# Optimization experiments

Hardware: AMD Instinct MI355X
Metric: run time of the kernel (lower is better)

## Reference

```python
import jax, jax.numpy as jnp
import numpy as np

D_IN = 2048
D_SAE = 32768
K = 64


def setup_inputs() -> dict:
    key = jax.random.key(0)
    k1, k2, k3 = jax.random.split(key, 3)
    x = jax.random.normal(k1, (4096, D_IN), dtype=jnp.float32)
    # kaiming-uniform-style init
    bound_enc = float(np.sqrt(6.0 / D_IN))
    W_enc = jax.random.uniform(k2, (D_SAE, D_IN), jnp.float32, -bound_enc, bound_enc)
    bound_dec = float(np.sqrt(6.0 / D_SAE))
    W_dec = jax.random.uniform(k3, (D_IN, D_SAE), jnp.float32, -bound_dec, bound_dec)
    # normalize_decoder: unit-norm columns of W_dec
    norms = jnp.clip(jnp.linalg.norm(W_dec, axis=0, keepdims=True), 1e-8, None)
    W_dec = W_dec / norms
    b_enc = jnp.zeros((D_SAE,), jnp.float32)
    b_dec = jnp.zeros((D_IN,), jnp.float32)
    return {"x": x, "W_enc": W_enc, "b_enc": b_enc, "W_dec": W_dec, "b_dec": b_dec}


def _topk_activate(pre_acts):
    # pre_acts: [N, d_sae] -> dense sparse activations with K nonzeros/row
    vals, idx = jax.lax.top_k(pre_acts, K)          # [N, K]
    vals = jax.nn.relu(vals)
    rows = jnp.arange(pre_acts.shape[0])[:, None]   # [N, 1]
    return jnp.zeros_like(pre_acts).at[rows, idx].set(vals)


def reference(x, W_enc, b_enc, W_dec, b_dec):
    # encode: activation(W_enc @ (x - b_dec) + b_enc)
    pre_acts = (x - b_dec) @ W_enc.T + b_enc        # [N, d_sae]
    h = _topk_activate(pre_acts)
    # decode
    x_hat = h @ W_dec.T + b_dec                     # [N, d_in]
    recon_loss = jnp.mean((x_hat - x) ** 2)
    loss = recon_loss  # topk: sparsity_loss == 0
    return (x_hat, h, loss)
```

## Files before the change

### kernel.cpp

```cpp
#include <hip/hip_runtime.h>
#include <stdint.h>

#define D_IN   2048
#define D_SAE  32768
#define NROWS  4096
#define TOPK   64
#define CAND_CAP 320
#define BMAX   96
#define CV_E   0.02f
#define TAU_COEF 0.0796875f
#define BINW   0.03125f

typedef __attribute__((ext_vector_type(4)))  float f32x4;
typedef __attribute__((ext_vector_type(8)))  short short8;
typedef __attribute__((ext_vector_type(4)))  unsigned short u16x4;
typedef __attribute__((ext_vector_type(8)))  unsigned short u16x8;

__device__ __forceinline__ unsigned short f2bf(float f){
  unsigned int u = __float_as_uint(f);
  u = (u + 0x7FFFu + ((u >> 16) & 1u)) >> 16;
  return (unsigned short)u;
}
__device__ __forceinline__ float bf2f(unsigned short h){
  return __uint_as_float(((unsigned int)h) << 16);
}
__device__ __forceinline__ void async16(const unsigned short* g, unsigned short* l){
  __builtin_amdgcn_global_load_lds(
      (const __attribute__((address_space(1))) unsigned int*)g,
      (__attribute__((address_space(3))) unsigned int*)l,
      16, 0, 0);
}

__global__ void __launch_bounds__(256) k_prep(
    const float* __restrict__ x, const float* __restrict__ b_dec,
    const float* __restrict__ W_enc,
    unsigned short* __restrict__ xbf, float* __restrict__ tau,
    int* __restrict__ cnt, unsigned short* __restrict__ wencb)
{
  const int t = threadIdx.x;
  if (blockIdx.x < NROWS){
    __shared__ float red[256];
    const int n = blockIdx.x;
    const f32x4* xr = (const f32x4*)(x + (size_t)n*D_IN);
    const f32x4* br = (const f32x4*)b_dec;
    u16x4* xo = (u16x4*)(xbf + (size_t)n*D_IN);
    float s = 0.f;
#pragma unroll
    for (int i=0;i<2;i++){
      const int p = t + 256*i;
      const f32x4 v = xr[p], b = br[p];
      f32x4 d; u16x4 r4;
#pragma unroll
      for (int j=0;j<4;j++){ d[j] = v[j]-b[j]; r4[j] = f2bf(d[j]); s = fmaf(d[j],d[j],s); }
      xo[p] = r4;
    }
    red[t] = s; __syncthreads();
    for (int o=128;o>0;o>>=1){ if (t<o) red[t] += red[t+o]; __syncthreads(); }
    if (t==0){ tau[n] = TAU_COEF * sqrtf(red[0]); cnt[n] = 0; }
  } else {
    const int i = (blockIdx.x - NROWS)*256 + t;
    const f32x4 v = ((const f32x4*)W_enc)[i];
    u16x4 r;
#pragma unroll
    for (int j=0;j<4;j++) r[j] = f2bf(v[j]);
    ((u16x4*)wencb)[i] = r;
  }
}

__global__ void __launch_bounds__(256) k_transpose(
    const float* __restrict__ wdec, unsigned short* __restrict__ wdt)
{
  __shared__ float tile[64][65];
  const int t = threadIdx.x;
  const int j0 = blockIdx.x*64;
  const int i0 = blockIdx.y*64;
  const int r = t >> 2, cq = (t & 3) * 16;
  const float* src = wdec + (size_t)(i0 + r)*D_SAE + j0 + cq;
#pragma unroll
  for (int k=0;k<4;k++){
    const f32x4 v = ((const f32x4*)src)[k];
#pragma unroll
    for (int e=0;e<4;e++) tile[r][cq + 4*k + e] = v[e];
  }
  __syncthreads();
  u16x8 o0, o1;
#pragma unroll
  for (int e=0;e<8;e++){
    o0[e] = f2bf(tile[cq + e][r]);
    o1[e] = f2bf(tile[cq + 8 + e][r]);
  }
  unsigned short* dst = wdt + (size_t)(j0 + r)*D_IN + i0 + cq;
  ((u16x8*)dst)[0] = o0;
  ((u16x8*)dst)[1] = o1;
}

__global__ void __launch_bounds__(256) k_gemm(
    const unsigned short* __restrict__ A,
    const unsigned short* __restrict__ B,
    const float* __restrict__ b_enc,
    const float* __restrict__ tau,
    int* __restrict__ cnt, int* __restrict__ ci, float* __restrict__ cv)
{
  __shared__ unsigned short As[128*32];
  __shared__ unsigned short Bs[128*32];
  const int tid = threadIdx.x;
  const int w = tid >> 6, l = tid & 63;
  const int bm = blockIdx.x, bn = blockIdx.y;
  const size_t brow = (size_t)bm*128, bcol = (size_t)bn*128;
  const int wr = w >> 1, wc = w & 1;
  const int srow = tid >> 2;
  const int skk  = (tid & 3) * 8;
  const int fr = l & 15, fq = l >> 4;
  f32x4 acc[4][4] = {};
  const unsigned short* Ab = A + (brow + srow)*D_IN + skk;
  const unsigned short* Bb = B + (bcol + srow)*D_IN + skk;
  for (int kt = 0; kt < D_IN; kt += 32){
    __syncthreads();
    async16(Ab + kt,                 &As[w*512]);
    async16(Ab + (size_t)64*D_IN+kt, &As[2048 + w*512]);
    async16(Bb + kt,                 &Bs[w*512]);
    async16(Bb + (size_t)64*D_IN+kt, &Bs[2048 + w*512]);
    __syncthreads();
    short8 af[4], bf[4];
#pragma unroll
    for (int m=0;m<4;m++) af[m] = *(const short8*)&As[(wr*64 + m*16 + fr)*32 + fq*8];
#pragma unroll
    for (int n=0;n<4;n++) bf[n] = *(const short8*)&Bs[(wc*64 + n*16 + fr)*32 + fq*8];
#pragma unroll
    for (int m=0;m<4;m++)
#pragma unroll
      for (int n=0;n<4;n++)
        asm("v_mfma_f32_16x16x32_bf16 %0, %1, %2, %0" : "+v"(acc[m][n]) : "v"(af[m]), "v"(bf[n]));
  }
  asm volatile("s_nop 7\n\ts_nop 7" ::: "memory");
#pragma unroll
  for (int n=0;n<4;n++){
    const int col = (int)bcol + wc*64 + n*16 + fr;
    const float be = b_enc[col];
#pragma unroll
    for (int m=0;m<4;m++){
      const int row0 = (int)brow + wr*64 + m*16 + fq*4;
#pragma unroll
      for (int r=0;r<4;r++){
        const float v = acc[m][n][r] + be;
        const int row = row0 + r;
        if (v > tau[row]){
          const int pos = atomicAdd(&cnt[row], 1);
          if (pos < CAND_CAP){
            ci[(size_t)row*CAND_CAP + pos] = col;
            cv[(size_t)row*CAND_CAP + pos] = v;
          }
        }
      }
    }
  }
}

__global__ void __launch_bounds__(256) k_rescore(
    const float* __restrict__ x, const float* __restrict__ b_dec,
    const float* __restrict__ W, const float* __restrict__ b_enc,
    const float* __restrict__ tau, const int* __restrict__ cnt,
    const int* __restrict__ ci, const float* __restrict__ cv,
    const unsigned short* __restrict__ wdt,
    float* __restrict__ h, float* __restrict__ xhat, double* __restrict__ part)
{
  __shared__ f32x4 xa[D_IN/4];
  __shared__ float sval[CAND_CAP];
  __shared__ int   sidx[CAND_CAP];
  __shared__ unsigned hist[256];
  __shared__ unsigned tsuf[256];
  __shared__ float osv[TOPK];
  __shared__ int   osi[TOPK];
  __shared__ float exv[BMAX];
  __shared__ int   exi[BMAX];
  __shared__ int   blist[BMAX];
  __shared__ int   m1c, m2c, sbin;
  const int n = blockIdx.x, t = threadIdx.x, w = t>>6, l = t&63;

  {
    const f32x4* xr = (const f32x4*)(x + (size_t)n*D_IN);
    const f32x4* br = (const f32x4*)b_dec;
    for (int i=t;i<D_IN/4;i+=256){
      f32x4 v = xr[i], b = br[i], d;
      d[0]=v[0]-b[0]; d[1]=v[1]-b[1]; d[2]=v[2]-b[2]; d[3]=v[3]-b[3];
      xa[i] = d;
    }
  }
  {
    f32x4* hr = (f32x4*)(h + (size_t)n*D_SAE);
    f32x4 z = {0.f,0.f,0.f,0.f};
#pragma unroll
    for (int i=0;i<32;i++) hr[t + 256*i] = z;
  }
  if (t < TOPK){ osv[t] = 0.f; osi[t] = 0; }
  hist[t] = 0u;
  if (t == 0){ m1c = 0; m2c = 0; sbin = 0; }
  int cn = cnt[n]; cn = cn < CAND_CAP ? cn : CAND_CAP;
  const float tn = tau[n];
  __syncthreads();
  for (int c=t; c<cn; c+=256){
    const float v = cv[(size_t)n*CAND_CAP + c];
    sval[c] = v;
    sidx[c] = ci[(size_t)n*CAND_CAP + c];
    int b = (int)((v - tn)*32.f); b = b<0?0:(b>255?255:b);
    atomicAdd(&hist[b], 1u);
  }
  __syncthreads();

  if (cn <= TOPK){
    for (int c=t; c<cn; c+=256){
      const int p = atomicAdd(&m1c, 1);
      osv[p] = sval[c]; osi[p] = sidx[c];
    }
    __syncthreads();
  } else {
    tsuf[t] = hist[t]; __syncthreads();
    for (int off=1; off<256; off<<=1){
      unsigned v = tsuf[t] + ((t+off<256)? tsuf[t+off] : 0u);
      __syncthreads();
      tsuf[t] = v;
      __syncthreads();
    }
    if (tsuf[t] >= (unsigned)TOPK) atomicMax(&sbin, t);
    __syncthreads();
    const int bT = sbin;
    const float THI = tn + (float)(bT+1)*BINW + 2.f*CV_E;
    const float TLO = tn + (float)bT*BINW     - 2.f*CV_E;
    for (int c=t; c<cn; c+=256){
      const float v = sval[c];
      if (v > THI){
        const int p = atomicAdd(&m1c, 1);
        osv[p] = v; osi[p] = sidx[c];
      } else if (v >= TLO){
        const int p = atomicAdd(&m2c, 1);
        if (p < BMAX) blist[p] = c;
      }
    }
    __syncthreads();
    const int m1 = m1c;
    const int m2 = m2c < BMAX ? m2c : BMAX;
    for (int c0 = w*2; c0 < m2; c0 += 8){
      const int c1 = c0 + 1;
      const int i0 = sidx[blist[c0]];
      const int i1 = (c1 < m2) ? sidx[blist[c1]] : i0;
      const f32x4* w0 = (const f32x4*)(W + (size_t)i0*D_IN);
      const f32x4* w1 = (const f32x4*)(W + (size_t)i1*D_IN);
      f32x4 a0 = {0.f,0.f,0.f,0.f}, a1 = {0.f,0.f,0.f,0.f};
#pragma unroll
      for (int e=0;e<8;e++){
        const int p = l + e*64;
        const f32x4 xv = xa[p];
        const f32x4 wv0 = w0[p];
        const f32x4 wv1 = w1[p];
#pragma unroll
        for (int j=0;j<4;j++) a0[j] = fmaf(xv[j], wv0[j], a0[j]);
#pragma unroll
        for (int j=0;j<4;j++) a1[j] = fmaf(xv[j], wv1[j], a1[j]);
      }
      float s0 = (a0[0]+a0[1]) + (a0[2]+a0[3]);
      float s1 = (a1[0]+a1[1]) + (a1[2]+a1[3]);
#pragma unroll
      for (int off=32; off>0; off>>=1){
        s0 += __shfl_down(s0, off);
        s1 += __shfl_down(s1, off);
      }
      if (l==0){
        exv[c0] = s0 + b_enc[i0]; exi[c0] = i0;
        if (c1 < m2){ exv[c1] = s1 + b_enc[i1]; exi[c1] = i1; }
      }
    }
    __syncthreads();
    if (w==0){
      const int need = TOPK - m1;
      for (int k=0;k<need;k++){
        float bv = -2.0e30f; int bi = 0x7FFFFFFF; int bp = -1;
        for (int c=l; c<m2; c+=64){
          const float v = exv[c]; const int idx = exi[c];
          if (v > bv || (v == bv && idx < bi)){ bv = v; bi = idx; bp = c; }
        }
#pragma unroll
        for (int off=32; off>0; off>>=1){
          const float ovv = __shfl_down(bv, off);
          const int   oii = __shfl_down(bi, off);
          const int   opp = __shfl_down(bp, off);
          if (ovv > bv || (ovv == bv && oii < bi)){ bv=ovv; bi=oii; bp=opp; }
        }
        bv = __shfl(bv, 0); bi = __shfl(bi, 0); bp = __shfl(bp, 0);
        if (l==0 && bp >= 0){
          osv[m1+k] = bv; osi[m1+k] = bi;
          exv[bp] = -3.0e30f;
        }
      }
    }
    __syncthreads();
  }
  if (t < TOPK){
    const float v = osv[t];
    if (v > 0.f) h[(size_t)n*D_SAE + osi[t]] = v;
  }
  __syncthreads();
  {
    const int d0 = t*8;
    float s[8] = {0.f,0.f,0.f,0.f,0.f,0.f,0.f,0.f};
    for (int k=0;k<TOPK;k++){
      const float v = osv[k];
      const u16x8 wv = *(const u16x8*)(wdt + (size_t)osi[k]*D_IN + d0);
#pragma unroll
      for (int j=0;j<8;j++) s[j] = fmaf(v, bf2f(wv[j]), s[j]);
    }
    const float* xaf = (const float*)xa;
    const f32x4 b0 = ((const f32x4*)b_dec)[t*2];
    const f32x4 b1 = ((const f32x4*)b_dec)[t*2+1];
    f32x4 o0, o1;
#pragma unroll
    for (int j=0;j<4;j++){ o0[j] = s[j] + b0[j]; o1[j] = s[j+4] + b1[j]; }
    float* xo = xhat + (size_t)n*D_IN + d0;
    ((f32x4*)xo)[0] = o0; ((f32x4*)xo)[1] = o1;
    float sq = 0.f;
#pragma unroll
    for (int j=0;j<8;j++){ const float d = s[j] - xaf[d0+j]; sq = fmaf(d,d,sq); }
    __syncthreads();
    sval[t] = sq; __syncthreads();
    for (int o=128;o>0;o>>=1){ if (t<o) sval[t] += sval[t+o]; __syncthreads(); }
    if (t==0) part[n] = (double)sval[0];
  }
}

__global__ void k_loss(const double* __restrict__ part, float* __restrict__ out){
  __shared__ double red[256];
  const int t = threadIdx.x;
  double a = 0.0;
  for (int i=t;i<NROWS;i+=256) a += part[i];
  red[t] = a; __syncthreads();
  for (int s=128;s>0;s>>=1){ if (t<s) red[t]+=red[t+s]; __syncthreads(); }
  if (t==0) out[0] = (float)(red[0] / (double)((size_t)NROWS * D_IN));
}

extern "C" void kernel_launch(void* const* d_in, const int* in_sizes, int n_in,
                              void* d_out, int out_size, void* d_ws, size_t ws_size,
                              hipStream_t stream)
{
  const float* x     = (const float*)d_in[0];
  const float* W_enc = (const float*)d_in[1];
  const float* b_enc = (const float*)d_in[2];
  const float* W_dec = (const float*)d_in[3];
  const float* b_dec = (const float*)d_in[4];

  float* xhat = (float*)d_out;
  float* h    = xhat + (size_t)NROWS*D_IN;
  float* loss = h + (size_t)NROWS*D_SAE;

  char* ws = (char*)d_ws;
  unsigned short* xbf   = (unsigned short*)(ws);
  unsigned short* wencb = (unsigned short*)(ws + 16777216);
  unsigned short* wdt   = (unsigned short*)(ws + 150994944);
  int*   ci   = (int*)  (ws + 285212672);
  float* cv   = (float*)(ws + 290455552);
  int*   cnt  = (int*)  (ws + 295698432);
  float* tau  = (float*)(ws + 295714816);
  double* part= (double*)(ws + 295731200);

  k_prep      <<<dim3(69632),   dim3(256), 0, stream>>>(x, b_dec, W_enc, xbf, tau, cnt, wencb);
  k_transpose <<<dim3(512,32),  dim3(256), 0, stream>>>(W_dec, wdt);
  k_gemm      <<<dim3(32,256),  dim3(256), 0, stream>>>(xbf, wencb, b_enc, tau, cnt, ci, cv);
  k_rescore   <<<dim3(4096),    dim3(256), 0, stream>>>(x, b_dec, W_enc, b_enc, tau, cnt, ci, cv, wdt, h, xhat, part);
  k_loss      <<<dim3(1),       dim3(256), 0, stream>>>(part, loss);
}
```

Before: 1.152 ms.

## Double GEMM K-tile to 64 with XOR-swizzled LDS layout

The encoder GEMM now stages a 64-wide K slice per iteration instead of 32, which halves the number of barrier pairs and global-to-LDS rounds. The LDS tiles are stored with an XOR swizzle of the 16-byte chunk index by row, so the MFMA fragment reads avoid bank conflicts. The cost is doubled shared memory per block, which may reduce occupancy, and more fragment registers live per iteration.

```diff
diff --git a/kernel.cpp b/kernel.cpp
--- a/kernel.cpp
+++ b/kernel.cpp
@@ -101,36 +101,46 @@
     const float* __restrict__ tau,
     int* __restrict__ cnt, int* __restrict__ ci, float* __restrict__ cv)
 {
-  __shared__ unsigned short As[128*32];
-  __shared__ unsigned short Bs[128*32];
+  __shared__ unsigned short As[128*64];
+  __shared__ unsigned short Bs[128*64];
   const int tid = threadIdx.x;
   const int w = tid >> 6, l = tid & 63;
   const int bm = blockIdx.x, bn = blockIdx.y;
   const size_t brow = (size_t)bm*128, bcol = (size_t)bn*128;
   const int wr = w >> 1, wc = w & 1;
-  const int srow = tid >> 2;
-  const int skk  = (tid & 3) * 8;
+  const int lr = l >> 3;
+  const int lg = (l & 7) ^ lr;
   const int fr = l & 15, fq = l >> 4;
+  const int fx = fr & 7;
   f32x4 acc[4][4] = {};
-  const unsigned short* Ab = A + (brow + srow)*D_IN + skk;
-  const unsigned short* Bb = B + (bcol + srow)*D_IN + skk;
-  for (int kt = 0; kt < D_IN; kt += 32){
-    __syncthreads();
-    async16(Ab + kt,                 &As[w*512]);
-    async16(Ab + (size_t)64*D_IN+kt, &As[2048 + w*512]);
-    async16(Bb + kt,                 &Bs[w*512]);
-    async16(Bb + (size_t)64*D_IN+kt, &Bs[2048 + w*512]);
-    __syncthreads();
-    short8 af[4], bf[4];
-#pragma unroll
-    for (int m=0;m<4;m++) af[m] = *(const short8*)&As[(wr*64 + m*16 + fr)*32 + fq*8];
-#pragma unroll
-    for (int n=0;n<4;n++) bf[n] = *(const short8*)&Bs[(wc*64 + n*16 + fr)*32 + fq*8];
+  const unsigned short* Ab = A + (brow + 8*w + lr)*D_IN + lg*8;
+  const unsigned short* Bb = B + (bcol + 8*w + lr)*D_IN + lg*8;
+  for (int kt = 0; kt < D_IN; kt += 64){
+    __syncthreads();
+#pragma unroll
+    for (int c=0;c<4;c++){
+      async16(Ab + (size_t)(32*c)*D_IN + kt, &As[c*2048 + w*512]);
+      async16(Bb + (size_t)(32*c)*D_IN + kt, &Bs[c*2048 + w*512]);
+    }
+    __syncthreads();
+    short8 af[4][2], bf[4][2];
 #pragma unroll
     for (int m=0;m<4;m++)
 #pragma unroll
-      for (int n=0;n<4;n++)
-        asm("v_mfma_f32_16x16x32_bf16 %0, %1, %2, %0" : "+v"(acc[m][n]) : "v"(af[m]), "v"(bf[n]));
+      for (int kk=0;kk<2;kk++)
+        af[m][kk] = *(const short8*)&As[(wr*64 + m*16 + fr)*64 + (((kk*4+fq) ^ fx)*8)];
+#pragma unroll
+    for (int n=0;n<4;n++)
+#pragma unroll
+      for (int kk=0;kk<2;kk++)
+        bf[n][kk] = *(const short8*)&Bs[(wc*64 + n*16 + fr)*64 + (((kk*4+fq) ^ fx)*8)];
+#pragma unroll
+    for (int kk=0;kk<2;kk++)
+#pragma unroll
+      for (int m=0;m<4;m++)
+#pragma unroll
+        for (int n=0;n<4;n++)
+          asm("v_mfma_f32_16x16x32_bf16 %0, %1, %2, %0" : "+v"(acc[m][n]) : "v"(af[m][kk]), "v"(bf[n][kk]));
   }
   asm volatile("s_nop 7\n\ts_nop 7" ::: "memory");
 #pragma unroll
```

Result: faster. 1.048 ms (-9.0%).
